# Performance work log

Measured on AMD Instinct MI355X. Metric: run time of the kernel, lower is better.

Reference implementation:

```python
import jax, jax.numpy as jnp
import numpy as np

NUM_LABELS = 1000
HIDDEN = 512
BATCH = 65536
NOISE_STD = 0.1
L_STAB, L_CENTER, L_SEP, L_BRIER = 1.0, 0.1, 0.01, 1.0


def setup_inputs() -> dict:
    key = jax.random.key(0)
    k1, k2, k3, k4, k5 = jax.random.split(key, 5)
    cls_rep = jax.random.normal(k1, (BATCH, HIDDEN), dtype=jnp.float32)
    logits = jax.random.normal(k2, (BATCH, NUM_LABELS), dtype=jnp.float32)
    labels = jax.random.randint(k3, (BATCH,), 0, NUM_LABELS)
    W = jax.random.normal(k4, (HIDDEN, NUM_LABELS), dtype=jnp.float32) * 0.02
    b = jnp.zeros((NUM_LABELS,), dtype=jnp.float32)
    noise = jax.random.normal(k5, (BATCH, HIDDEN), dtype=jnp.float32)
    centers = jnp.zeros((NUM_LABELS, HIDDEN), dtype=jnp.float32)
    return {"cls_rep": cls_rep, "logits": logits, "labels": labels,
            "W": W, "b": b, "noise": noise, "centers": centers}


def _compute_all(cls_rep, logits, labels, W, b, noise, centers):
    # --- update_centers (init branch, no_grad): per-class mean via segment_sum ---
    ones = jnp.ones((cls_rep.shape[0],), dtype=cls_rep.dtype)
    counts = jax.ops.segment_sum(ones, labels, num_segments=NUM_LABELS)           # [C]
    sums = jax.ops.segment_sum(cls_rep, labels, num_segments=NUM_LABELS)          # [C, H]
    present = counts > 0
    batch_means = sums / jnp.maximum(counts, 1.0)[:, None]
    new_centers = jnp.where(present[:, None], batch_means, centers)               # [C, H]
    new_centers = jax.lax.stop_gradient(new_centers)

    # --- stability: classifier(cls_rep + noise_std * eps) vs clean logits ---
    logits_noisy = (cls_rep + NOISE_STD * noise) @ W + b                          # [B, C]
    stab = jnp.mean((logits_noisy - logits) ** 2)

    # --- center loss: gather centroids, MSE ---
    center = jnp.mean((cls_rep - new_centers[labels]) ** 2)

    # --- separation: cdist + exp, minus exp(0)*num_labels ---
    sq = jnp.sum(new_centers ** 2, axis=1)                                        # [C]
    d2 = jnp.maximum(sq[:, None] + sq[None, :] - 2.0 * new_centers @ new_centers.T, 0.0)
    dist = jnp.sqrt(d2)                                                           # [C, C]
    I = jnp.eye(NUM_LABELS, dtype=dist.dtype)
    sep = jnp.sum(jnp.exp(-dist + I)) - jnp.float32(NUM_LABELS)

    # --- brier: softmax vs one-hot ---
    probs = jax.nn.softmax(logits, axis=-1)
    one_hot = jax.nn.one_hot(labels, NUM_LABELS, dtype=logits.dtype)
    brier = jnp.mean(jnp.sum((probs - one_hot) ** 2, axis=1))

    total = L_STAB * stab + L_CENTER * center + L_SEP * sep + L_BRIER * brier
    return jnp.stack([total, stab, center, sep, brier])


def reference(cls_rep, logits, labels, W, b, noise, centers):
    return _compute_all(cls_rep, logits, labels, W, b, noise, centers)
```

## Files before the change

### kernel.cpp

```cpp
#include <hip/hip_runtime.h>

#define BATCH 65536
#define HID   512
#define NCLS  1000
#define NCLSP 1024

typedef long i64;
typedef float f32x4 __attribute__((ext_vector_type(4)));
typedef float f32x2 __attribute__((ext_vector_type(2)));
typedef unsigned short u16;
typedef unsigned int u32;
typedef unsigned char u8;

__device__ __forceinline__ u16 f2bf(float f) {
  u32 u = __float_as_uint(f);
  u += 0x7fffu + ((u >> 16) & 1u);
  return (u16)(u >> 16);
}

__device__ __forceinline__ u32 pk4(float a, float b, float c, float d) {
  u32 r = 0;
  r = (u32)__builtin_amdgcn_cvt_pk_fp8_f32(a, b, (int)r, false);
  r = (u32)__builtin_amdgcn_cvt_pk_fp8_f32(c, d, (int)r, true);
  return r;
}
__device__ __forceinline__ u8 pk1(float a) {
  return (u8)(__builtin_amdgcn_cvt_pk_fp8_f32(a, 0.f, 0, false) & 0xff);
}

#define WS_END 2899968

__global__ void k_zero(int* __restrict__ counts, double* __restrict__ accum) {
  const int t = threadIdx.x;
  counts[t] = 0;
  if (t < 8) accum[t] = 0.0;
}

__global__ void k_hist(const int* __restrict__ labels, int* __restrict__ counts) {
  const int i = blockIdx.x * blockDim.x + threadIdx.x;
  if (i < BATCH) atomicAdd(counts + labels[i], 1);
}

__global__ void k_scan(const int* __restrict__ counts, int* __restrict__ offsets) {
  __shared__ int tmp[1024];
  const int t = threadIdx.x;
  const int v = counts[t];
  tmp[t] = v;
  __syncthreads();
  for (int d = 1; d < 1024; d <<= 1) {
    int u = (t >= d) ? tmp[t - d] : 0;
    __syncthreads();
    tmp[t] += u;
    __syncthreads();
  }
  offsets[t] = tmp[t] - v;
}

__global__ void k_scatter(const int* __restrict__ labels, int* __restrict__ offsets,
                          int* __restrict__ order) {
  const int i = blockIdx.x * blockDim.x + threadIdx.x;
  if (i < BATCH) {
    const int pos = atomicAdd(offsets + labels[i], 1);
    order[pos] = i;
  }
}

__global__ void k_segsum(const float* __restrict__ cls, const int* __restrict__ order,
                         const int* __restrict__ offsets, const int* __restrict__ counts,
                         const float* __restrict__ cen_in, float* __restrict__ cen,
                         float* __restrict__ sq, double* __restrict__ accum) {
  __shared__ float red[8];
  __shared__ float redc[8];
  const int c = blockIdx.x;
  const int t = threadIdx.x;
  const int cnt = counts[c];
  const int end = offsets[c];
  const int start = end - cnt;
  float v, cp;
  if (cnt > 0) {
    float s0 = 0.f, s1 = 0.f, s2 = 0.f, s3 = 0.f;
    float q0 = 0.f, q1 = 0.f, q2 = 0.f, q3 = 0.f;
    int i = start;
    for (; i + 4 <= end; i += 4) {
      const int r0 = order[i], r1 = order[i + 1], r2 = order[i + 2], r3 = order[i + 3];
      float x0 = cls[(size_t)r0 * HID + t];
      float x1 = cls[(size_t)r1 * HID + t];
      float x2 = cls[(size_t)r2 * HID + t];
      float x3 = cls[(size_t)r3 * HID + t];
      s0 += x0; q0 = fmaf(x0, x0, q0);
      s1 += x1; q1 = fmaf(x1, x1, q1);
      s2 += x2; q2 = fmaf(x2, x2, q2);
      s3 += x3; q3 = fmaf(x3, x3, q3);
    }
    for (; i < end; ++i) {
      float x = cls[(size_t)order[i] * HID + t];
      s0 += x; q0 = fmaf(x, x, q0);
    }
    v = ((s0 + s1) + (s2 + s3)) / (float)cnt;
    cp = ((q0 + q1) + (q2 + q3)) - (float)cnt * v * v;
  } else {
    v = (c < NCLS) ? cen_in[(size_t)c * HID + t] : 0.f;
    cp = 0.f;
  }
  cen[(size_t)c * HID + t] = v;

  float p = v * v;
  #pragma unroll
  for (int s = 32; s; s >>= 1) { p += __shfl_xor(p, s); cp += __shfl_xor(cp, s); }
  if ((t & 63) == 0) { red[t >> 6] = p; redc[t >> 6] = cp; }
  __syncthreads();
  if (t == 0) {
    float acc = 0.f, accc = 0.f;
    #pragma unroll
    for (int i = 0; i < 8; ++i) { acc += red[i]; accc += redc[i]; }
    sq[c] = acc;
    atomicAdd(accum + 1, (double)accc);
  }
}

__global__ void k_wconv(const float* __restrict__ W, u32* __restrict__ wb) {
  const int j = blockIdx.x * blockDim.x + threadIdx.x;
  const int kc = j >> 13, col = (j >> 3) & 1023, kg = (j >> 1) & 3, i0 = (j & 1) * 4;
  const int k = kc * 32 + kg * 8 + i0;
  float w0 = 0.f, w1 = 0.f, w2 = 0.f, w3 = 0.f;
  if (col < NCLS) {
    w0 = W[(size_t)(k + 0) * NCLS + col] * 16.f;
    w1 = W[(size_t)(k + 1) * NCLS + col] * 16.f;
    w2 = W[(size_t)(k + 2) * NCLS + col] * 16.f;
    w3 = W[(size_t)(k + 3) * NCLS + col] * 16.f;
  }
  wb[j] = pk4(w0, w1, w2, w3);
}

__global__ void k_sep(const float* __restrict__ cen, const float* __restrict__ sq,
                      double* __restrict__ accum) {
  __shared__ float As[16][64];
  __shared__ float Bs[16][64];
  __shared__ float red[4];
  const int bi = blockIdx.x >> 4, bj = blockIdx.x & 15;
  const int tx = threadIdx.x & 15, ty = threadIdx.x >> 4;
  const int lrow = threadIdx.x & 63, lkq = threadIdx.x >> 6;
  float acc[4][4] = {};
  for (int k0 = 0; k0 < HID; k0 += 16) {
    __syncthreads();
    float4 a = *(const float4*)(cen + (size_t)(bi * 64 + lrow) * HID + k0 + lkq * 4);
    float4 b = *(const float4*)(cen + (size_t)(bj * 64 + lrow) * HID + k0 + lkq * 4);
    As[lkq*4+0][lrow] = a.x; As[lkq*4+1][lrow] = a.y; As[lkq*4+2][lrow] = a.z; As[lkq*4+3][lrow] = a.w;
    Bs[lkq*4+0][lrow] = b.x; Bs[lkq*4+1][lrow] = b.y; Bs[lkq*4+2][lrow] = b.z; Bs[lkq*4+3][lrow] = b.w;
    __syncthreads();
    #pragma unroll
    for (int k = 0; k < 16; ++k) {
      float4 av = *(const float4*)&As[k][ty * 4];
      float4 bv = *(const float4*)&Bs[k][tx * 4];
      float ar[4] = {av.x, av.y, av.z, av.w};
      float br[4] = {bv.x, bv.y, bv.z, bv.w};
      #pragma unroll
      for (int r = 0; r < 4; ++r)
        #pragma unroll
        for (int s = 0; s < 4; ++s)
          acc[r][s] = fmaf(ar[r], br[s], acc[r][s]);
    }
  }
  float part = 0.f;
  #pragma unroll
  for (int r = 0; r < 4; ++r) {
    const int i = bi * 64 + ty * 4 + r;
    #pragma unroll
    for (int s = 0; s < 4; ++s) {
      const int j = bj * 64 + tx * 4 + s;
      if (i < NCLS && j < NCLS) {
        float d2 = fmaxf(sq[i] + sq[j] - 2.f * acc[r][s], 0.f);
        float dist = sqrtf(d2);
        part += __expf((i == j ? 1.f : 0.f) - dist);
      }
    }
  }
  #pragma unroll
  for (int s = 32; s; s >>= 1) part += __shfl_xor(part, s);
  if ((threadIdx.x & 63) == 0) red[threadIdx.x >> 6] = part;
  __syncthreads();
  if (threadIdx.x == 0)
    atomicAdd(accum + 2, (double)(red[0] + red[1] + red[2] + red[3]));
}

__global__ __launch_bounds__(1024, 8)
void k_gemm(const float* __restrict__ cls, const float* __restrict__ noise,
            const float* __restrict__ logits, const int* __restrict__ labels,
            const float* __restrict__ bias, const u8* __restrict__ wb,
            double* __restrict__ accum) {
  __shared__ u8 Apan[32 * 512];
  __shared__ u8 lntile[32 * 1024];
  __shared__ float redf[32];
  const int lane = threadIdx.x & 63;
  const int w = threadIdx.x >> 6;
  const int row0 = blockIdx.x * 32;
  const int l15 = lane & 15, lkg = lane >> 4;

  {
    const int row_loc = threadIdx.x >> 5;
    const int k0 = (threadIdx.x & 31) * 16;
    const int sw = ((row_loc & 7) << 3) | (((row_loc >> 3) & 1) << 6);
    const float* cp = cls   + (size_t)(row0 + row_loc) * HID;
    const float* np = noise + (size_t)(row0 + row_loc) * HID;
    #pragma unroll
    for (int q = 0; q < 2; ++q) {
      const int g = k0 + q * 8;
      const int k = g ^ sw;
      float4 a0 = *(const float4*)(cp + k), a1 = *(const float4*)(cp + k + 4);
      float4 n0 = *(const float4*)(np + k), n1 = *(const float4*)(np + k + 4);
      uint2 p;
      p.x = pk4(fmaf(0.1f, n0.x, a0.x), fmaf(0.1f, n0.y, a0.y),
                fmaf(0.1f, n0.z, a0.z), fmaf(0.1f, n0.w, a0.w));
      p.y = pk4(fmaf(0.1f, n1.x, a1.x), fmaf(0.1f, n1.y, a1.y),
                fmaf(0.1f, n1.z, a1.z), fmaf(0.1f, n1.w, a1.w));
      *(uint2*)&Apan[row_loc * 512 + g] = p;
    }
  }
  __syncthreads();

  f32x4 acc[2][4] = {};
  const int swr = ((l15 & 7) << 3) | ((l15 >> 3) << 6);
  const u8* bb0 = wb + (w * 64 + l15) * 32 + lkg * 8;
  i64 bcur[4];
  #pragma unroll
  for (int ct = 0; ct < 4; ++ct) bcur[ct] = *(const i64*)(bb0 + ct * 512);
  for (int kc = 0; kc < 16; ++kc) {
    const int kn = (kc < 15) ? kc + 1 : 15;
    const u8* bbn = bb0 + (size_t)kn * 32768;
    i64 bnxt[4];
    #pragma unroll
    for (int ct = 0; ct < 4; ++ct) bnxt[ct] = *(const i64*)(bbn + ct * 512);
    i64 af0 = *(const i64*)&Apan[(l15)      * 512 + ((kc * 32 + lkg * 8) ^ swr)];
    i64 af1 = *(const i64*)&Apan[(16 + l15) * 512 + ((kc * 32 + lkg * 8) ^ swr)];
    #pragma unroll
    for (int ct = 0; ct < 4; ++ct) {
      acc[0][ct] = __builtin_amdgcn_mfma_f32_16x16x32_fp8_fp8(af0, bcur[ct], acc[0][ct], 0, 0, 0);
      acc[1][ct] = __builtin_amdgcn_mfma_f32_16x16x32_fp8_fp8(af1, bcur[ct], acc[1][ct], 0, 0, 0);
    }
    #pragma unroll
    for (int ct = 0; ct < 4; ++ct) bcur[ct] = bnxt[ct];
  }

  #pragma unroll
  for (int ct = 0; ct < 4; ++ct) {
    const int col = w * 64 + ct * 16 + l15;
    if (col < NCLS) {
      const float bc = bias[col];
      #pragma unroll
      for (int rt = 0; rt < 2; ++rt) {
        #pragma unroll
        for (int r = 0; r < 4; ++r) {
          const int rowloc = rt * 16 + lkg * 4 + r;
          lntile[rowloc * 1024 + (col ^ ((rowloc & 12) << 2))] =
              pk1(fmaf(acc[rt][ct][r], 0.0625f, bc));
        }
      }
    }
  }
  __syncthreads();

  float spart = 0.f, bpart = 0.f;
  #pragma unroll
  for (int j = 0; j < 2; ++j) {
    const int rowloc = w * 2 + j;
    const int row = row0 + rowloc;
    const int swz = (rowloc & 12) << 2;
    const u8* lnrow = lntile + rowloc * 1024;
    const float4* lr = (const float4*)(logits + (size_t)row * NCLS);
    const int lab2 = labels[row];
    const float el = __expf(logits[(size_t)row * NCLS + lab2]);
    float S = 0.f, S2 = 0.f;
    #pragma unroll
    for (int it = 0; it < 4; ++it) {
      const int f = it * 64 + lane;
      if (f < 250) {
        float4 lg = lr[f];
        u32 v = *(const u32*)(lnrow + ((f * 4) ^ swz));
        f32x2 lo = __builtin_amdgcn_cvt_pk_f32_fp8((int)v, false);
        f32x2 hi = __builtin_amdgcn_cvt_pk_f32_fp8((int)v, true);
        float d0 = lo[0] - lg.x, d1 = lo[1] - lg.y, d2 = hi[0] - lg.z, d3 = hi[1] - lg.w;
        spart += d0 * d0 + d1 * d1 + d2 * d2 + d3 * d3;
        float e0 = __expf(lg.x), e1 = __expf(lg.y), e2 = __expf(lg.z), e3 = __expf(lg.w);
        S += e0 + e1 + e2 + e3;
        S2 += e0 * e0 + e1 * e1 + e2 * e2 + e3 * e3;
      }
    }
    #pragma unroll
    for (int s = 32; s; s >>= 1) { S += __shfl_xor(S, s); S2 += __shfl_xor(S2, s); }
    bpart += S2 / (S * S) - 2.f * el / S + 1.f;
  }
  #pragma unroll
  for (int s = 32; s; s >>= 1) { spart += __shfl_xor(spart, s); bpart += __shfl_xor(bpart, s); }

  if (lane == 0) { redf[w] = spart; redf[16 + w] = bpart; }
  __syncthreads();
  if (threadIdx.x == 0) {
    float st = 0.f, br = 0.f;
    #pragma unroll
    for (int i = 0; i < 16; ++i) { st += redf[i]; br += redf[16 + i]; }
    atomicAdd(accum + 0, (double)st);
    atomicAdd(accum + 3, (double)br);
  }
}

__global__ void k_final(const double* __restrict__ accum, float* __restrict__ out) {
  if (threadIdx.x == 0) {
    double stab   = accum[0] / ((double)BATCH * (double)NCLS);
    double center = accum[1] / ((double)BATCH * (double)HID);
    double sep    = accum[2] - (double)NCLS;
    double brier  = accum[3] / (double)BATCH;
    double total  = 1.0 * stab + 0.1 * center + 0.01 * sep + 1.0 * brier;
    out[0] = (float)total;
    out[1] = (float)stab;
    out[2] = (float)center;
    out[3] = (float)sep;
    out[4] = (float)brier;
  }
}

extern "C" void kernel_launch(void* const* d_in, const int* in_sizes, int n_in,
                              void* d_out, int out_size, void* d_ws, size_t ws_size,
                              hipStream_t stream) {
  const float* cls    = (const float*)d_in[0];
  const float* logits = (const float*)d_in[1];
  const int*   labels = (const int*)d_in[2];
  const float* W      = (const float*)d_in[3];
  const float* bias   = (const float*)d_in[4];
  const float* noise  = (const float*)d_in[5];
  const float* cen_in = (const float*)d_in[6];
  float* out = (float*)d_out;
  char* ws = (char*)d_ws;
  if (ws_size < (size_t)WS_END) return;

  int*    counts  = (int*)(ws + 0);
  double* accum   = (double*)(ws + 4096);
  float*  sq      = (float*)(ws + 8192);
  int*    offsets = (int*)(ws + 12288);
  int*    order   = (int*)(ws + 16384);
  float*  cen     = (float*)(ws + 278528);
  u8*     wb8     = (u8*)(ws + 2375680);

  hipLaunchKernelGGL(k_zero,    dim3(1),    dim3(1024),0, stream, counts, accum);
  hipLaunchKernelGGL(k_hist,    dim3(256),  dim3(256), 0, stream, labels, counts);
  hipLaunchKernelGGL(k_wconv,   dim3(512),  dim3(256), 0, stream, W, (u32*)wb8);
  hipLaunchKernelGGL(k_scan,    dim3(1),    dim3(1024),0, stream, counts, offsets);
  hipLaunchKernelGGL(k_scatter, dim3(256),  dim3(256), 0, stream, labels, offsets, order);
  hipLaunchKernelGGL(k_segsum,  dim3(1024), dim3(512), 0, stream, cls, order, offsets, counts, cen_in, cen, sq, accum);
  hipLaunchKernelGGL(k_sep,     dim3(256),  dim3(256), 0, stream, cen, sq, accum);
  hipLaunchKernelGGL(k_gemm,    dim3(2048), dim3(1024), 0, stream, cls, noise, logits, labels, bias, wb8, accum);
  hipLaunchKernelGGL(k_final,   dim3(1),    dim3(64),  0, stream, accum, out);
}
```

Baseline: 255.9 us.

## Fuse segment-sum center computation into the GEMM kernel via interleaved block roles

Removes the separate k_segsum launch and folds its work into the big GEMM kernel. Every fifth block, with two 512-thread halves, computes two class centers, and the other four blocks per group of five do GEMM row tiles. The aim is to drop a kernel launch boundary and let the gather-heavy segment sums overlap with the MFMA-bound GEMM work. k_sep now runs after the fused kernel, so it still sees the centers. The segsum blocks pay for the GEMM kernel's large shared-memory footprint and 1024-thread shape, which may limit occupancy for them.

```diff
diff --git a/kernel.cpp b/kernel.cpp
--- a/kernel.cpp
+++ b/kernel.cpp
@@ -12,12 +12,6 @@
 typedef unsigned int u32;
 typedef unsigned char u8;
 
-__device__ __forceinline__ u16 f2bf(float f) {
-  u32 u = __float_as_uint(f);
-  u += 0x7fffu + ((u >> 16) & 1u);
-  return (u16)(u >> 16);
-}
-
 __device__ __forceinline__ u32 pk4(float a, float b, float c, float d) {
   u32 r = 0;
   r = (u32)__builtin_amdgcn_cvt_pk_fp8_f32(a, b, (int)r, false);
@@ -62,59 +56,6 @@
   if (i < BATCH) {
     const int pos = atomicAdd(offsets + labels[i], 1);
     order[pos] = i;
-  }
-}
-
-__global__ void k_segsum(const float* __restrict__ cls, const int* __restrict__ order,
-                         const int* __restrict__ offsets, const int* __restrict__ counts,
-                         const float* __restrict__ cen_in, float* __restrict__ cen,
-                         float* __restrict__ sq, double* __restrict__ accum) {
-  __shared__ float red[8];
-  __shared__ float redc[8];
-  const int c = blockIdx.x;
-  const int t = threadIdx.x;
-  const int cnt = counts[c];
-  const int end = offsets[c];
-  const int start = end - cnt;
-  float v, cp;
-  if (cnt > 0) {
-    float s0 = 0.f, s1 = 0.f, s2 = 0.f, s3 = 0.f;
-    float q0 = 0.f, q1 = 0.f, q2 = 0.f, q3 = 0.f;
-    int i = start;
-    for (; i + 4 <= end; i += 4) {
-      const int r0 = order[i], r1 = order[i + 1], r2 = order[i + 2], r3 = order[i + 3];
-      float x0 = cls[(size_t)r0 * HID + t];
-      float x1 = cls[(size_t)r1 * HID + t];
-      float x2 = cls[(size_t)r2 * HID + t];
-      float x3 = cls[(size_t)r3 * HID + t];
-      s0 += x0; q0 = fmaf(x0, x0, q0);
-      s1 += x1; q1 = fmaf(x1, x1, q1);
-      s2 += x2; q2 = fmaf(x2, x2, q2);
-      s3 += x3; q3 = fmaf(x3, x3, q3);
-    }
-    for (; i < end; ++i) {
-      float x = cls[(size_t)order[i] * HID + t];
-      s0 += x; q0 = fmaf(x, x, q0);
-    }
-    v = ((s0 + s1) + (s2 + s3)) / (float)cnt;
-    cp = ((q0 + q1) + (q2 + q3)) - (float)cnt * v * v;
-  } else {
-    v = (c < NCLS) ? cen_in[(size_t)c * HID + t] : 0.f;
-    cp = 0.f;
-  }
-  cen[(size_t)c * HID + t] = v;
-
-  float p = v * v;
-  #pragma unroll
-  for (int s = 32; s; s >>= 1) { p += __shfl_xor(p, s); cp += __shfl_xor(cp, s); }
-  if ((t & 63) == 0) { red[t >> 6] = p; redc[t >> 6] = cp; }
-  __syncthreads();
-  if (t == 0) {
-    float acc = 0.f, accc = 0.f;
-    #pragma unroll
-    for (int i = 0; i < 8; ++i) { acc += red[i]; accc += redc[i]; }
-    sq[c] = acc;
-    atomicAdd(accum + 1, (double)accc);
   }
 }
 
@@ -184,16 +125,75 @@
 }
 
 __global__ __launch_bounds__(1024, 8)
-void k_gemm(const float* __restrict__ cls, const float* __restrict__ noise,
-            const float* __restrict__ logits, const int* __restrict__ labels,
-            const float* __restrict__ bias, const u8* __restrict__ wb,
-            double* __restrict__ accum) {
+void k_fat(const float* __restrict__ cls, const float* __restrict__ noise,
+           const float* __restrict__ logits, const int* __restrict__ labels,
+           const float* __restrict__ bias, const u8* __restrict__ wb,
+           const int* __restrict__ order, const int* __restrict__ offsets,
+           const int* __restrict__ counts, const float* __restrict__ cen_in,
+           float* __restrict__ cen, float* __restrict__ sq,
+           double* __restrict__ accum) {
   __shared__ u8 Apan[32 * 512];
   __shared__ u8 lntile[32 * 1024];
   __shared__ float redf[32];
+  __shared__ float sred[2][8];
+  __shared__ float sredc[2][8];
+
+  const int r5 = blockIdx.x % 5;
+  const int q5 = blockIdx.x / 5;
+
+  if (r5 == 4) {
+    const int half = threadIdx.x >> 9;
+    const int tt = threadIdx.x & 511;
+    const int c = q5 * 2 + half;
+    const int cnt = counts[c];
+    const int end = offsets[c];
+    const int start = end - cnt;
+    float v, cp;
+    if (cnt > 0) {
+      float s0 = 0.f, s1 = 0.f, s2 = 0.f, s3 = 0.f;
+      float q0 = 0.f, q1 = 0.f, q2 = 0.f, q3 = 0.f;
+      int i = start;
+      for (; i + 4 <= end; i += 4) {
+        const int r0 = order[i], r1 = order[i + 1], r2 = order[i + 2], r3 = order[i + 3];
+        float x0 = cls[(size_t)r0 * HID + tt];
+        float x1 = cls[(size_t)r1 * HID + tt];
+        float x2 = cls[(size_t)r2 * HID + tt];
+        float x3 = cls[(size_t)r3 * HID + tt];
+        s0 += x0; q0 = fmaf(x0, x0, q0);
+        s1 += x1; q1 = fmaf(x1, x1, q1);
+        s2 += x2; q2 = fmaf(x2, x2, q2);
+        s3 += x3; q3 = fmaf(x3, x3, q3);
+      }
+      for (; i < end; ++i) {
+        float x = cls[(size_t)order[i] * HID + tt];
+        s0 += x; q0 = fmaf(x, x, q0);
+      }
+      v = ((s0 + s1) + (s2 + s3)) / (float)cnt;
+      cp = ((q0 + q1) + (q2 + q3)) - (float)cnt * v * v;
+    } else {
+      v = (c < NCLS) ? cen_in[(size_t)c * HID + tt] : 0.f;
+      cp = 0.f;
+    }
+    cen[(size_t)c * HID + tt] = v;
+    float p = v * v;
+    #pragma unroll
+    for (int s = 32; s; s >>= 1) { p += __shfl_xor(p, s); cp += __shfl_xor(cp, s); }
+    if ((tt & 63) == 0) { sred[half][tt >> 6] = p; sredc[half][tt >> 6] = cp; }
+    __syncthreads();
+    if (tt == 0) {
+      float acc = 0.f, accc = 0.f;
+      #pragma unroll
+      for (int i = 0; i < 8; ++i) { acc += sred[half][i]; accc += sredc[half][i]; }
+      sq[c] = acc;
+      atomicAdd(accum + 1, (double)accc);
+    }
+    return;
+  }
+
+  const int gidx = q5 * 4 + r5;
   const int lane = threadIdx.x & 63;
   const int w = threadIdx.x >> 6;
-  const int row0 = blockIdx.x * 32;
+  const int row0 = gidx * 32;
   const int l15 = lane & 15, lkg = lane >> 4;
 
   {
@@ -345,8 +345,9 @@
   hipLaunchKernelGGL(k_wconv,   dim3(512),  dim3(256), 0, stream, W, (u32*)wb8);
   hipLaunchKernelGGL(k_scan,    dim3(1),    dim3(1024),0, stream, counts, offsets);
   hipLaunchKernelGGL(k_scatter, dim3(256),  dim3(256), 0, stream, labels, offsets, order);
-  hipLaunchKernelGGL(k_segsum,  dim3(1024), dim3(512), 0, stream, cls, order, offsets, counts, cen_in, cen, sq, accum);
+  hipLaunchKernelGGL(k_fat,     dim3(2560), dim3(1024), 0, stream,
+                     cls, noise, logits, labels, bias, wb8,
+                     order, offsets, counts, cen_in, cen, sq, accum);
   hipLaunchKernelGGL(k_sep,     dim3(256),  dim3(256), 0, stream, cen, sq, accum);
-  hipLaunchKernelGGL(k_gemm,    dim3(2048), dim3(1024), 0, stream, cls, noise, logits, labels, bias, wb8, accum);
   hipLaunchKernelGGL(k_final,   dim3(1),    dim3(64),  0, stream, accum, out);
 }
```

New measurement: 260.7 us. No clear change (+1.8%).

## Fuse histogram with weight conversion, vectorize segsum, widen sep blocks

Applied to the files above, without the earlier changes.

Merges the label histogram and the FP8 weight conversion into one launch, which saves a kernel launch. The segment-sum kernel now gives each row to one of four thread groups, loads float4 per thread, and reduces the groups through shared memory, so more rows are in flight per class. The separation kernel goes to 512 threads with a 2x4 register tile per thread to raise occupancy. These preprocessing kernels are small next to the main GEMM, so the overall effect is likely minor.

```diff
diff --git a/kernel.cpp b/kernel.cpp
--- a/kernel.cpp
+++ b/kernel.cpp
@@ -12,12 +12,6 @@
 typedef unsigned int u32;
 typedef unsigned char u8;
 
-__device__ __forceinline__ u16 f2bf(float f) {
-  u32 u = __float_as_uint(f);
-  u += 0x7fffu + ((u >> 16) & 1u);
-  return (u16)(u >> 16);
-}
-
 __device__ __forceinline__ u32 pk4(float a, float b, float c, float d) {
   u32 r = 0;
   r = (u32)__builtin_amdgcn_cvt_pk_fp8_f32(a, b, (int)r, false);
@@ -36,9 +30,25 @@
   if (t < 8) accum[t] = 0.0;
 }
 
-__global__ void k_hist(const int* __restrict__ labels, int* __restrict__ counts) {
-  const int i = blockIdx.x * blockDim.x + threadIdx.x;
-  if (i < BATCH) atomicAdd(counts + labels[i], 1);
+__global__ void k_hw(const int* __restrict__ labels, int* __restrict__ counts,
+                     const float* __restrict__ W, u32* __restrict__ wb) {
+  const int b = blockIdx.x;
+  if (b < 256) {
+    const int i = b * 256 + threadIdx.x;
+    if (i < BATCH) atomicAdd(counts + labels[i], 1);
+  } else {
+    const int j = (b - 256) * 256 + threadIdx.x;
+    const int kc = j >> 13, col = (j >> 3) & 1023, kg = (j >> 1) & 3, i0 = (j & 1) * 4;
+    const int k = kc * 32 + kg * 8 + i0;
+    float w0 = 0.f, w1 = 0.f, w2 = 0.f, w3 = 0.f;
+    if (col < NCLS) {
+      w0 = W[(size_t)(k + 0) * NCLS + col] * 16.f;
+      w1 = W[(size_t)(k + 1) * NCLS + col] * 16.f;
+      w2 = W[(size_t)(k + 2) * NCLS + col] * 16.f;
+      w3 = W[(size_t)(k + 3) * NCLS + col] * 16.f;
+    }
+    wb[j] = pk4(w0, w1, w2, w3);
+  }
 }
 
 __global__ void k_scan(const int* __restrict__ counts, int* __restrict__ offsets) {
@@ -65,122 +75,116 @@
   }
 }
 
-__global__ void k_segsum(const float* __restrict__ cls, const int* __restrict__ order,
-                         const int* __restrict__ offsets, const int* __restrict__ counts,
-                         const float* __restrict__ cen_in, float* __restrict__ cen,
-                         float* __restrict__ sq, double* __restrict__ accum) {
-  __shared__ float red[8];
-  __shared__ float redc[8];
+__global__ __launch_bounds__(512)
+void k_segsum(const float* __restrict__ cls, const int* __restrict__ order,
+              const int* __restrict__ offsets, const int* __restrict__ counts,
+              const float* __restrict__ cen_in, float* __restrict__ cen,
+              float* __restrict__ sq, double* __restrict__ accum) {
+  __shared__ float4 sm[512];
+  __shared__ float4 qm[512];
+  __shared__ float red[16];
   const int c = blockIdx.x;
   const int t = threadIdx.x;
+  const int cidx = t & 127;
+  const int rgrp = t >> 7;
   const int cnt = counts[c];
   const int end = offsets[c];
   const int start = end - cnt;
-  float v, cp;
-  if (cnt > 0) {
-    float s0 = 0.f, s1 = 0.f, s2 = 0.f, s3 = 0.f;
-    float q0 = 0.f, q1 = 0.f, q2 = 0.f, q3 = 0.f;
-    int i = start;
-    for (; i + 4 <= end; i += 4) {
-      const int r0 = order[i], r1 = order[i + 1], r2 = order[i + 2], r3 = order[i + 3];
-      float x0 = cls[(size_t)r0 * HID + t];
-      float x1 = cls[(size_t)r1 * HID + t];
-      float x2 = cls[(size_t)r2 * HID + t];
-      float x3 = cls[(size_t)r3 * HID + t];
-      s0 += x0; q0 = fmaf(x0, x0, q0);
-      s1 += x1; q1 = fmaf(x1, x1, q1);
-      s2 += x2; q2 = fmaf(x2, x2, q2);
-      s3 += x3; q3 = fmaf(x3, x3, q3);
-    }
-    for (; i < end; ++i) {
-      float x = cls[(size_t)order[i] * HID + t];
-      s0 += x; q0 = fmaf(x, x, q0);
-    }
-    v = ((s0 + s1) + (s2 + s3)) / (float)cnt;
-    cp = ((q0 + q1) + (q2 + q3)) - (float)cnt * v * v;
-  } else {
-    v = (c < NCLS) ? cen_in[(size_t)c * HID + t] : 0.f;
-    cp = 0.f;
-  }
-  cen[(size_t)c * HID + t] = v;
-
-  float p = v * v;
-  #pragma unroll
-  for (int s = 32; s; s >>= 1) { p += __shfl_xor(p, s); cp += __shfl_xor(cp, s); }
-  if ((t & 63) == 0) { red[t >> 6] = p; redc[t >> 6] = cp; }
+  float4 s = make_float4(0.f, 0.f, 0.f, 0.f);
+  float4 q = make_float4(0.f, 0.f, 0.f, 0.f);
+  for (int i = start + rgrp; i < end; i += 4) {
+    const float4 x = *(const float4*)(cls + (size_t)order[i] * HID + cidx * 4);
+    s.x += x.x; s.y += x.y; s.z += x.z; s.w += x.w;
+    q.x = fmaf(x.x, x.x, q.x); q.y = fmaf(x.y, x.y, q.y);
+    q.z = fmaf(x.z, x.z, q.z); q.w = fmaf(x.w, x.w, q.w);
+  }
+  sm[t] = s; qm[t] = q;
+  __syncthreads();
+  float p = 0.f, cp = 0.f;
+  if (t < 128) {
+    float4 S = sm[t], Q = qm[t];
+    float4 a = sm[128 + t], b = sm[256 + t], d = sm[384 + t];
+    S.x += a.x + b.x + d.x; S.y += a.y + b.y + d.y;
+    S.z += a.z + b.z + d.z; S.w += a.w + b.w + d.w;
+    a = qm[128 + t]; b = qm[256 + t]; d = qm[384 + t];
+    Q.x += a.x + b.x + d.x; Q.y += a.y + b.y + d.y;
+    Q.z += a.z + b.z + d.z; Q.w += a.w + b.w + d.w;
+    float4 v;
+    if (cnt > 0) {
+      const float fc = (float)cnt, inv = 1.f / fc;
+      v = make_float4(S.x * inv, S.y * inv, S.z * inv, S.w * inv);
+      cp = (Q.x - fc * v.x * v.x) + (Q.y - fc * v.y * v.y)
+         + (Q.z - fc * v.z * v.z) + (Q.w - fc * v.w * v.w);
+    } else {
+      v = (c < NCLS) ? *(const float4*)(cen_in + (size_t)c * HID + t * 4)
+                     : make_float4(0.f, 0.f, 0.f, 0.f);
+      cp = 0.f;
+    }
+    *(float4*)(cen + (size_t)c * HID + t * 4) = v;
+    p = v.x * v.x + v.y * v.y + v.z * v.z + v.w * v.w;
+  }
+  #pragma unroll
+  for (int sh = 32; sh; sh >>= 1) { p += __shfl_xor(p, sh); cp += __shfl_xor(cp, sh); }
+  if (t < 128 && (t & 63) == 0) { red[t >> 6] = p; red[8 + (t >> 6)] = cp; }
   __syncthreads();
   if (t == 0) {
-    float acc = 0.f, accc = 0.f;
-    #pragma unroll
-    for (int i = 0; i < 8; ++i) { acc += red[i]; accc += redc[i]; }
-    sq[c] = acc;
-    atomicAdd(accum + 1, (double)accc);
-  }
-}
-
-__global__ void k_wconv(const float* __restrict__ W, u32* __restrict__ wb) {
-  const int j = blockIdx.x * blockDim.x + threadIdx.x;
-  const int kc = j >> 13, col = (j >> 3) & 1023, kg = (j >> 1) & 3, i0 = (j & 1) * 4;
-  const int k = kc * 32 + kg * 8 + i0;
-  float w0 = 0.f, w1 = 0.f, w2 = 0.f, w3 = 0.f;
-  if (col < NCLS) {
-    w0 = W[(size_t)(k + 0) * NCLS + col] * 16.f;
-    w1 = W[(size_t)(k + 1) * NCLS + col] * 16.f;
-    w2 = W[(size_t)(k + 2) * NCLS + col] * 16.f;
-    w3 = W[(size_t)(k + 3) * NCLS + col] * 16.f;
-  }
-  wb[j] = pk4(w0, w1, w2, w3);
-}
-
-__global__ void k_sep(const float* __restrict__ cen, const float* __restrict__ sq,
-                      double* __restrict__ accum) {
+    sq[c] = red[0] + red[1];
+    atomicAdd(accum + 1, (double)(red[8] + red[9]));
+  }
+}
+
+__global__ __launch_bounds__(512)
+void k_sep(const float* __restrict__ cen, const float* __restrict__ sq,
+           double* __restrict__ accum) {
   __shared__ float As[16][64];
   __shared__ float Bs[16][64];
-  __shared__ float red[4];
+  __shared__ float red[8];
   const int bi = blockIdx.x >> 4, bj = blockIdx.x & 15;
   const int tx = threadIdx.x & 15, ty = threadIdx.x >> 4;
   const int lrow = threadIdx.x & 63, lkq = threadIdx.x >> 6;
-  float acc[4][4] = {};
+  float acc[2][4] = {};
   for (int k0 = 0; k0 < HID; k0 += 16) {
     __syncthreads();
-    float4 a = *(const float4*)(cen + (size_t)(bi * 64 + lrow) * HID + k0 + lkq * 4);
-    float4 b = *(const float4*)(cen + (size_t)(bj * 64 + lrow) * HID + k0 + lkq * 4);
-    As[lkq*4+0][lrow] = a.x; As[lkq*4+1][lrow] = a.y; As[lkq*4+2][lrow] = a.z; As[lkq*4+3][lrow] = a.w;
-    Bs[lkq*4+0][lrow] = b.x; Bs[lkq*4+1][lrow] = b.y; Bs[lkq*4+2][lrow] = b.z; Bs[lkq*4+3][lrow] = b.w;
+    f32x2 a = *(const f32x2*)(cen + (size_t)(bi * 64 + lrow) * HID + k0 + lkq * 2);
+    f32x2 b = *(const f32x2*)(cen + (size_t)(bj * 64 + lrow) * HID + k0 + lkq * 2);
+    As[lkq * 2 + 0][lrow] = a[0]; As[lkq * 2 + 1][lrow] = a[1];
+    Bs[lkq * 2 + 0][lrow] = b[0]; Bs[lkq * 2 + 1][lrow] = b[1];
     __syncthreads();
     #pragma unroll
     for (int k = 0; k < 16; ++k) {
-      float4 av = *(const float4*)&As[k][ty * 4];
-      float4 bv = *(const float4*)&Bs[k][tx * 4];
-      float ar[4] = {av.x, av.y, av.z, av.w};
-      float br[4] = {bv.x, bv.y, bv.z, bv.w};
-      #pragma unroll
-      for (int r = 0; r < 4; ++r)
-        #pragma unroll
-        for (int s = 0; s < 4; ++s)
-          acc[r][s] = fmaf(ar[r], br[s], acc[r][s]);
+      const float a0 = As[k][ty];
+      const float a1 = As[k][ty + 32];
+      const float4 bv = *(const float4*)&Bs[k][tx * 4];
+      acc[0][0] = fmaf(a0, bv.x, acc[0][0]); acc[0][1] = fmaf(a0, bv.y, acc[0][1]);
+      acc[0][2] = fmaf(a0, bv.z, acc[0][2]); acc[0][3] = fmaf(a0, bv.w, acc[0][3]);
+      acc[1][0] = fmaf(a1, bv.x, acc[1][0]); acc[1][1] = fmaf(a1, bv.y, acc[1][1]);
+      acc[1][2] = fmaf(a1, bv.z, acc[1][2]); acc[1][3] = fmaf(a1, bv.w, acc[1][3]);
     }
   }
   float part = 0.f;
   #pragma unroll
-  for (int r = 0; r < 4; ++r) {
-    const int i = bi * 64 + ty * 4 + r;
-    #pragma unroll
-    for (int s = 0; s < 4; ++s) {
-      const int j = bj * 64 + tx * 4 + s;
+  for (int r = 0; r < 2; ++r) {
+    const int i = bi * 64 + ty + r * 32;
+    #pragma unroll
+    for (int s2 = 0; s2 < 4; ++s2) {
+      const int j = bj * 64 + tx * 4 + s2;
       if (i < NCLS && j < NCLS) {
-        float d2 = fmaxf(sq[i] + sq[j] - 2.f * acc[r][s], 0.f);
+        float d2 = fmaxf(sq[i] + sq[j] - 2.f * acc[r][s2], 0.f);
         float dist = sqrtf(d2);
         part += __expf((i == j ? 1.f : 0.f) - dist);
       }
     }
   }
   #pragma unroll
-  for (int s = 32; s; s >>= 1) part += __shfl_xor(part, s);
+  for (int sh = 32; sh; sh >>= 1) part += __shfl_xor(part, sh);
   if ((threadIdx.x & 63) == 0) red[threadIdx.x >> 6] = part;
   __syncthreads();
-  if (threadIdx.x == 0)
-    atomicAdd(accum + 2, (double)(red[0] + red[1] + red[2] + red[3]));
+  if (threadIdx.x == 0) {
+    float acc8 = 0.f;
+    #pragma unroll
+    for (int i = 0; i < 8; ++i) acc8 += red[i];
+    atomicAdd(accum + 2, (double)acc8);
+  }
 }
 
 __global__ __launch_bounds__(1024, 8)
@@ -340,13 +344,12 @@
   float*  cen     = (float*)(ws + 278528);
   u8*     wb8     = (u8*)(ws + 2375680);
 
-  hipLaunchKernelGGL(k_zero,    dim3(1),    dim3(1024),0, stream, counts, accum);
-  hipLaunchKernelGGL(k_hist,    dim3(256),  dim3(256), 0, stream, labels, counts);
-  hipLaunchKernelGGL(k_wconv,   dim3(512),  dim3(256), 0, stream, W, (u32*)wb8);
-  hipLaunchKernelGGL(k_scan,    dim3(1),    dim3(1024),0, stream, counts, offsets);
-  hipLaunchKernelGGL(k_scatter, dim3(256),  dim3(256), 0, stream, labels, offsets, order);
-  hipLaunchKernelGGL(k_segsum,  dim3(1024), dim3(512), 0, stream, cls, order, offsets, counts, cen_in, cen, sq, accum);
-  hipLaunchKernelGGL(k_sep,     dim3(256),  dim3(256), 0, stream, cen, sq, accum);
+  hipLaunchKernelGGL(k_zero,    dim3(1),    dim3(1024), 0, stream, counts, accum);
+  hipLaunchKernelGGL(k_hw,      dim3(768),  dim3(256),  0, stream, labels, counts, W, (u32*)wb8);
+  hipLaunchKernelGGL(k_scan,    dim3(1),    dim3(1024), 0, stream, counts, offsets);
+  hipLaunchKernelGGL(k_scatter, dim3(256),  dim3(256),  0, stream, labels, offsets, order);
+  hipLaunchKernelGGL(k_segsum,  dim3(1024), dim3(512),  0, stream, cls, order, offsets, counts, cen_in, cen, sq, accum);
+  hipLaunchKernelGGL(k_sep,     dim3(256),  dim3(512),  0, stream, cen, sq, accum);
   hipLaunchKernelGGL(k_gemm,    dim3(2048), dim3(1024), 0, stream, cls, noise, logits, labels, bias, wb8, accum);
-  hipLaunchKernelGGL(k_final,   dim3(1),    dim3(64),  0, stream, accum, out);
-}
+  hipLaunchKernelGGL(k_final,   dim3(1),    dim3(64),   0, stream, accum, out);
+}
```

New measurement: 263.0 us. +2.8%, slower.
